# Kernel tuning notes

Hardware: AMD Instinct MI355X
Metric: run time of the kernel (lower is better)

## Reference

```python
import jax, jax.numpy as jnp
import numpy as np

EPS = 1e-5

def setup_inputs() -> dict:
    key = jax.random.key(0)
    k1, k2, k3 = jax.random.split(key, 3)
    x = jax.random.normal(k1, (16, 256, 32, 32), dtype=jnp.float32)
    embed = jax.random.normal(k2, (8192, 256), dtype=jnp.float32)
    cluster_size = jax.random.uniform(k3, (8192,), dtype=jnp.float32)
    return {"x": x, "embed": embed, "cluster_size": cluster_size}

def reference(x, embed, cluster_size):
    # x: (b, c, h, w) -> (b, h*w, c); project_in is Identity (codebook_dim == dim, heads=1)
    b, c, h, w = x.shape
    xt = jnp.transpose(x, (0, 2, 3, 1)).reshape(b, h * w, c)   # (b, n, d)
    flat = xt.reshape(-1, c)                                    # (N, d)
    d2 = (jnp.sum(flat * flat, axis=1, keepdims=True)
          - 2.0 * flat @ embed.T
          + jnp.sum(embed * embed, axis=1))                     # (N, K)
    embed_ind_flat = jnp.argmin(d2, axis=-1)                    # (N,) temperature==0 -> argmax of -d2
    quantize = embed[embed_ind_flat].reshape(b, h * w, c)       # gather codebook rows
    embed_ind = embed_ind_flat.reshape(b, h * w)
    # perplexity over (unnormalized) EMA cluster sizes, as in the torch code
    probs = cluster_size
    perplexity = jnp.exp(-jnp.sum(probs * jnp.log(probs + EPS)))
    # eval-mode commitment loss (weight_loss=True, commitment_weight=1.0)
    commit_loss = jnp.mean((quantize - xt) ** 2)
    return quantize, embed_ind, perplexity, commit_loss
```

## Files before the change

kernel.cpp:

```cpp
#include <hip/hip_runtime.h>
#include <hip/hip_bf16.h>
#include <math.h>

typedef _Float16 f16x8 __attribute__((ext_vector_type(8)));
typedef float f32x4 __attribute__((ext_vector_type(4)));

#define N_TOK 16384
#define D 256
#define K 8192

#define Q_OFF 0
#define IND_OFF 4194304
#define PERP_OFF 4210688
#define COMMIT_OFF 4210689

#define WS_CAND   0u
#define WS_E2     1048576u
#define WS_DSUM   1081344u
#define WS_EH     1114112u
#define WS_XH     5308416u
#define WS_XT     13697024u
#define WS_NEED   30474240u

__device__ __forceinline__ unsigned int ford(float f) {
    unsigned int u = __float_as_uint(f);
    return (u & 0x80000000u) ? ~u : (u | 0x80000000u);
}
__device__ __forceinline__ unsigned short f2h(float f) {
    _Float16 h = (_Float16)f;
    return *(unsigned short*)&h;
}


__global__ void vq_convert_x(const float* __restrict__ x, float* __restrict__ xt,
                             unsigned short* __restrict__ xh) {
    __shared__ float t[64][65];
    const int tid = threadIdx.x;
    const int p0 = blockIdx.x * 64, c0 = blockIdx.y * 64, b = blockIdx.z;
    const int q = tid & 15, h = tid >> 4;
    #pragma unroll
    for (int r = 0; r < 4; ++r) {
        const int cl = r * 16 + h;
        const float4 v = *(const float4*)(x + (((size_t)(b * 256 + c0 + cl)) << 10) + p0 + q * 4);
        t[cl][q * 4 + 0] = v.x; t[cl][q * 4 + 1] = v.y;
        t[cl][q * 4 + 2] = v.z; t[cl][q * 4 + 3] = v.w;
    }
    __syncthreads();
    #pragma unroll
    for (int r = 0; r < 4; ++r) {
        const int nl = r * 16 + h;
        const int n = (b << 10) + p0 + nl;
        const int c = c0 + q * 4;
        float4 vf; ushort4 vh;
        vf.x = t[q * 4 + 0][nl]; vf.y = t[q * 4 + 1][nl];
        vf.z = t[q * 4 + 2][nl]; vf.w = t[q * 4 + 3][nl];
        vh.x = f2h(vf.x); vh.y = f2h(vf.y); vh.z = f2h(vf.z); vh.w = f2h(vf.w);
        *(float4*)(xt + ((size_t)n << 8) + c) = vf;
        *(ushort4*)(xh + ((size_t)n << 8) + c) = vh;
    }
}

__global__ void vq_prep_e(const float* __restrict__ e, unsigned short* __restrict__ ehT,
                          float* __restrict__ e2, double* __restrict__ dsum) {
    if (blockIdx.x == 0 && threadIdx.x == 0) *dsum = 0.0;
    const int wave = threadIdx.x >> 6, lane = threadIdx.x & 63;
    const int c = blockIdx.x * 4 + wave;
    const float4 v = *(const float4*)(e + (size_t)c * D + lane * 4);
    ushort4 vh;
    vh.x = f2h(v.x); vh.y = f2h(v.y); vh.z = f2h(v.z); vh.w = f2h(v.w);
    unsigned short* dst = ehT + (((size_t)(c >> 4)) << 12) + ((lane >> 1) << 7) +
                          ((c & 15) << 3) + ((lane & 1) << 2);
    *(ushort4*)dst = vh;
    float s = v.x * v.x + v.y * v.y + v.z * v.z + v.w * v.w;
    #pragma unroll
    for (int off = 32; off > 0; off >>= 1) s += __shfl_down(s, off, 64);
    if (lane == 0) e2[c] = s;
}

__global__ __launch_bounds__(256)
void vq_mfma_kernel(
    const unsigned short* __restrict__ xh, const unsigned short* __restrict__ ehT,
    const float* __restrict__ e2, unsigned int* __restrict__ cand) {
    __shared__ float e2s[1024];

    const int tid = threadIdx.x;
    const int lane = tid & 63, wid = tid >> 6;
    const int l15 = lane & 15, lg = lane >> 4;
    const int split = blockIdx.y;
    const int m0 = blockIdx.x * 128;
    const int c0s = split * 1024;
    const int rw = m0 + wid * 32;

    {
        float4 v = *(const float4*)(e2 + c0s + tid * 4);
        v.x += 512.0f; v.y += 512.0f; v.z += 512.0f; v.w += 512.0f;
        *(float4*)&e2s[tid * 4] = v;
    }

    f16x8 a[2][8];
    #pragma unroll
    for (int mf = 0; mf < 2; ++mf) {
        const unsigned short* ap = xh + (((size_t)(rw + mf * 16 + l15)) << 8) + lg * 8;
        #pragma unroll
        for (int t = 0; t < 8; ++t)
            a[mf][t] = *(const f16x8*)(ap + t * 32);
    }
    __syncthreads();

    const char* bb = (const char*)ehT + (((size_t)c0s) << 9) + lane * 16;

    unsigned int p1[8], p2[8];
    #pragma unroll
    for (int r = 0; r < 8; ++r) { p1[r] = 0xFFFFFFFFu; p2[r] = 0xFFFFFFFFu; }

    f16x8 bA[8], bB[8];
    f32x4 accA[2], accB[2];

#define LOADT(breg, t)                                            \
    {                                                             \
        const char* tb_ = bb + (t) * 8192;                        \
        _Pragma("unroll")                                         \
        for (int j_ = 0; j_ < 8; ++j_)                            \
            breg[j_] = *(const f16x8*)(tb_ + j_ * 1024);          \
    }

#define MFMAT(acc, breg)                                          \
    {                                                             \
        _Pragma("unroll")                                         \
        for (int mf_ = 0; mf_ < 2; ++mf_) {                       \
            f32x4 z_ = {0.f, 0.f, 0.f, 0.f};                      \
            acc[mf_] = z_;                                        \
        }                                                         \
        _Pragma("unroll")                                         \
        for (int j_ = 0; j_ < 8; ++j_)                            \
            _Pragma("unroll")                                     \
            for (int mf_ = 0; mf_ < 2; ++mf_)                     \
                acc[mf_] = __builtin_amdgcn_mfma_f32_16x16x32_f16(\
                    a[mf_][j_], breg[j_], acc[mf_], 0, 0, 0);     \
    }

#define EPI(acc, tile)                                                        \
    {                                                                         \
        const float e2v_ = e2s[(tile) * 16 + l15];                            \
        const unsigned int cl_ = (unsigned int)((tile) * 16 + l15);           \
        _Pragma("unroll")                                                     \
        for (int mf_ = 0; mf_ < 2; ++mf_)                                     \
            _Pragma("unroll")                                                 \
            for (int rg_ = 0; rg_ < 4; ++rg_) {                               \
                const int rr_ = mf_ * 4 + rg_;                                \
                const float s_ = fmaf(-2.0f, acc[mf_][rg_], e2v_);            \
                const unsigned int sp_ =                                      \
                    (__float_as_uint(s_) & 0xFFFFFC00u) | cl_;                \
                const unsigned int hi_ = p1[rr_] > sp_ ? p1[rr_] : sp_;       \
                p1[rr_] = p1[rr_] < sp_ ? p1[rr_] : sp_;                      \
                p2[rr_] = p2[rr_] < hi_ ? p2[rr_] : hi_;                      \
            }                                                                 \
    }

    LOADT(bA, 0);
    #pragma unroll 1
    for (int t = 0; t < 64; t += 2) {
        LOADT(bB, t + 1);
        MFMAT(accA, bA);
        if (t > 0) EPI(accB, t - 1);
        if (t + 2 < 64) LOADT(bA, t + 2);
        MFMAT(accB, bB);
        EPI(accA, t);
    }
    EPI(accB, 63);

    #pragma unroll
    for (int st = 1; st < 16; st <<= 1) {
        #pragma unroll
        for (int r = 0; r < 8; ++r) {
            const unsigned int q1 = (unsigned int)__shfl_xor((int)p1[r], st, 64);
            const unsigned int q2 = (unsigned int)__shfl_xor((int)p2[r], st, 64);
            const unsigned int n1 = p1[r] < q1 ? p1[r] : q1;
            const unsigned int hi = p1[r] < q1 ? q1 : p1[r];
            const unsigned int m2 = p2[r] < q2 ? p2[r] : q2;
            p1[r] = n1;
            p2[r] = m2 < hi ? m2 : hi;
        }
    }
    if (l15 == 0) {
        #pragma unroll
        for (int mf = 0; mf < 2; ++mf)
            #pragma unroll
            for (int reg = 0; reg < 4; ++reg) {
                const int rr = mf * 4 + reg;
                const int n = rw + mf * 16 + lg * 4 + reg;
                unsigned int* cp = cand + (((size_t)n) << 4) + split * 2;
                cp[0] = (unsigned int)(c0s + (p1[rr] & 0x3FFu));
                cp[1] = (unsigned int)(c0s + (p2[rr] & 0x3FFu));
            }
    }
#undef LOADT
#undef MFMAT
#undef EPI
}

__global__ void vq_rescore_finalize(const float* __restrict__ xt, const float* __restrict__ embed,
                                    const float* __restrict__ e2,
                                    const unsigned int* __restrict__ cand,
                                    float* __restrict__ out, double* __restrict__ dsum) {
    __shared__ double red[4];
    const int tid = threadIdx.x, wid = tid >> 6, lane = tid & 63;
    double wsum = 0.0;
    #pragma unroll 1
    for (int it = 0; it < 4; ++it) {
        const int n = blockIdx.x * 16 + it * 4 + wid;
        const float4 xv = *(const float4*)(xt + (((size_t)n) << 8) + lane * 4);
        unsigned long long best = 0xFFFFFFFFFFFFFFFFull;
        #pragma unroll 2
        for (int j = 0; j < 16; ++j) {
            const unsigned int c = cand[(((size_t)n) << 4) + j];
            const float4 ev = *(const float4*)(embed + (((size_t)c) << 8) + lane * 4);
            float dt = xv.x * ev.x + xv.y * ev.y + xv.z * ev.z + xv.w * ev.w;
            #pragma unroll
            for (int off = 32; off > 0; off >>= 1) dt += __shfl_xor(dt, off, 64);
            const float s = fmaf(-2.0f, dt, e2[c]);
            const unsigned long long p = (((unsigned long long)ford(s)) << 32) | c;
            best = p < best ? p : best;
        }
        const unsigned int bi = (unsigned int)(best & 0xFFFFFFFFull);
        if (lane == 0) out[IND_OFF + n] = (float)bi;
        const float4 ev = *(const float4*)(embed + (((size_t)bi) << 8) + lane * 4);
        *(float4*)(out + Q_OFF + (((size_t)n) << 8) + lane * 4) = ev;
        const float q0 = ev.x - xv.x, q1 = ev.y - xv.y, q2 = ev.z - xv.z, q3 = ev.w - xv.w;
        float a4 = q0 * q0 + q1 * q1 + q2 * q2 + q3 * q3;
        #pragma unroll
        for (int off = 32; off > 0; off >>= 1) a4 += __shfl_xor(a4, off, 64);
        if (lane == 0) wsum += (double)a4;
    }
    if (lane == 0) red[wid] = wsum;
    __syncthreads();
    if (tid == 0) atomicAdd(dsum, red[0] + red[1] + red[2] + red[3]);
}

__global__ void vq_tail_kernel(const float* __restrict__ cs,
                               const double* __restrict__ dsum,
                               float* __restrict__ out) {
    __shared__ double red[4];
    const int tid = threadIdx.x;
    double s = 0.0;
    for (int i = tid; i < K; i += 256) {
        const float p = cs[i];
        s += (double)(p * logf(p + 1e-5f));
    }
    #pragma unroll
    for (int off = 32; off > 0; off >>= 1) s += __shfl_down(s, off, 64);
    if ((tid & 63) == 0) red[tid >> 6] = s;
    __syncthreads();
    if (tid == 0) {
        const double tot = red[0] + red[1] + red[2] + red[3];
        const double pv = exp(-tot);
        out[PERP_OFF] = (pv > 3.3e38) ? 3.3e38f : (float)pv;
        out[COMMIT_OFF] = (float)(*dsum * (1.0 / 4194304.0));
    }
}

#define TM 64
#define TN 64
#define BKF 32
#define NSPLITF 2
#define CODES_PER_SPLIT (K / NSPLITF)
#define TILES_PER_SPLIT (CODES_PER_SPLIT / TN)

__global__ void vq_init_kernel(unsigned long long* __restrict__ keys, double* __restrict__ dsum) {
    int i = blockIdx.x * blockDim.x + threadIdx.x;
    if (i < N_TOK) keys[i] = 0xFFFFFFFFFFFFFFFFull;
    if (i == 0) *dsum = 0.0;
}
__global__ void vq_e2_kernel(const float* __restrict__ embed, float* __restrict__ e2) {
    int wave = threadIdx.x >> 6, lane = threadIdx.x & 63;
    int c = blockIdx.x * 4 + wave;
    const float4 v = *(const float4*)(embed + (size_t)c * D + lane * 4);
    float s = v.x * v.x + v.y * v.y + v.z * v.z + v.w * v.w;
    #pragma unroll
    for (int off = 32; off > 0; off >>= 1) s += __shfl_down(s, off, 64);
    if (lane == 0) e2[c] = s;
}
__global__ __launch_bounds__(256, 2) void vq_argmin_kernel(
    const float* __restrict__ x, const float* __restrict__ embed,
    const float* __restrict__ e2, unsigned long long* __restrict__ keys) {
    __shared__ float xT[D][TM];
    __shared__ float eT[BKF][TN + 4];
    const int tid = threadIdx.x;
    const int n0 = blockIdx.x * TM;
    const int b = n0 >> 10, p0 = n0 & 1023;
    const float* xb = x + (size_t)b * D * 1024 + p0;
    {
        const int t4 = (tid & 15) * 4, chb = tid >> 4;
        #pragma unroll
        for (int pass = 0; pass < 16; ++pass) {
            const int ch = pass * 16 + chb;
            *(float4*)&xT[ch][t4] = *(const float4*)(xb + (size_t)ch * 1024 + t4);
        }
    }
    __syncthreads();
    const int tm4 = (tid & 15) * 4, tn = tid >> 4, tn4 = tn * 4;
    float bestd[4]; int besti[4];
    #pragma unroll
    for (int i = 0; i < 4; ++i) { bestd[i] = INFINITY; besti[i] = 0x7fffffff; }
    for (int ct = 0; ct < TILES_PER_SPLIT; ++ct) {
        const int c0 = blockIdx.y * CODES_PER_SPLIT + ct * TN;
        float acc[4][4] = {};
        for (int kk = 0; kk < D; kk += BKF) {
            {
                const int j = tid >> 2, ch4 = (tid & 3) * 4;
                #pragma unroll
                for (int p = 0; p < 2; ++p) {
                    const int chl = p * 16 + ch4;
                    const float4 ev = *(const float4*)(embed + (size_t)(c0 + j) * D + kk + chl);
                    eT[chl + 0][j] = ev.x; eT[chl + 1][j] = ev.y;
                    eT[chl + 2][j] = ev.z; eT[chl + 3][j] = ev.w;
                }
            }
            __syncthreads();
            #pragma unroll
            for (int k2 = 0; k2 < BKF; ++k2) {
                const float4 a = *(const float4*)&xT[kk + k2][tm4];
                const float4 bv = *(const float4*)&eT[k2][tn4];
                acc[0][0] += a.x * bv.x; acc[0][1] += a.x * bv.y; acc[0][2] += a.x * bv.z; acc[0][3] += a.x * bv.w;
                acc[1][0] += a.y * bv.x; acc[1][1] += a.y * bv.y; acc[1][2] += a.y * bv.z; acc[1][3] += a.y * bv.w;
                acc[2][0] += a.z * bv.x; acc[2][1] += a.z * bv.y; acc[2][2] += a.z * bv.z; acc[2][3] += a.z * bv.w;
                acc[3][0] += a.w * bv.x; acc[3][1] += a.w * bv.y; acc[3][2] += a.w * bv.z; acc[3][3] += a.w * bv.w;
            }
            __syncthreads();
        }
        #pragma unroll
        for (int j = 0; j < 4; ++j) {
            const int c = c0 + tn4 + j;
            const float ec = e2[c];
            #pragma unroll
            for (int i = 0; i < 4; ++i) {
                const float s = ec - 2.0f * acc[i][j];
                if (s < bestd[i]) { bestd[i] = s; besti[i] = c; }
            }
        }
    }
    __syncthreads();
    float* cd = &eT[0][0];
    int* ci = (int*)&eT[16][0];
    #pragma unroll
    for (int i = 0; i < 4; ++i) { cd[tn * 64 + tm4 + i] = bestd[i]; ci[tn * 64 + tm4 + i] = besti[i]; }
    __syncthreads();
    if (tid < TM) {
        float bd = INFINITY; int bi = 0x7fffffff;
        for (int j = 0; j < 16; ++j) {
            const float d = cd[j * 64 + tid]; const int idx = ci[j * 64 + tid];
            if (d < bd || (d == bd && idx < bi)) { bd = d; bi = idx; }
        }
        atomicMin(&keys[n0 + tid], (((unsigned long long)ford(bd)) << 32) | (unsigned int)bi);
    }
}
__global__ void vq_finalize_kernel(const float* __restrict__ x, const float* __restrict__ embed,
                                   const unsigned long long* __restrict__ keys,
                                   float* __restrict__ out, double* __restrict__ dsum) {
    const int tid = threadIdx.x;
    const int n0 = blockIdx.x * 64;
    const int t = tid >> 2, q = tid & 3;
    const int n = n0 + t;
    const int b = n >> 10, p = n & 1023;
    if (tid < 64) {
        const int nn = n0 + tid;
        out[IND_OFF + nn] = (float)(int)(unsigned int)(keys[nn] & 0xFFFFFFFFull);
    }
    const int idx = (int)(unsigned int)(keys[n] & 0xFFFFFFFFull);
    const float* erow = embed + (size_t)idx * D;
    const float* xrow = x + (size_t)b * D * 1024 + p;
    float* qrow = out + Q_OFF + (size_t)n * D;
    float acc = 0.0f;
    #pragma unroll
    for (int i = 0; i < 16; ++i) {
        const int ch = i * 16 + q * 4;
        const float4 ev = *(const float4*)(erow + ch);
        *(float4*)(qrow + ch) = ev;
        const float x0 = xrow[(size_t)(ch + 0) * 1024];
        const float x1 = xrow[(size_t)(ch + 1) * 1024];
        const float x2 = xrow[(size_t)(ch + 2) * 1024];
        const float x3 = xrow[(size_t)(ch + 3) * 1024];
        const float d0 = ev.x - x0, d1 = ev.y - x1, d2 = ev.z - x2, d3 = ev.w - x3;
        acc += d0 * d0 + d1 * d1 + d2 * d2 + d3 * d3;
    }
    #pragma unroll
    for (int off = 32; off > 0; off >>= 1) acc += __shfl_down(acc, off, 64);
    if ((tid & 63) == 0) atomicAdd(dsum, (double)acc);
}

extern "C" void kernel_launch(void* const* d_in, const int* in_sizes, int n_in,
                              void* d_out, int out_size, void* d_ws, size_t ws_size,
                              hipStream_t stream) {
    const float* x = (const float*)d_in[0];
    const float* embed = (const float*)d_in[1];
    const float* cs = (const float*)d_in[2];
    float* out = (float*)d_out;
    char* ws = (char*)d_ws;

    if (ws_size >= (size_t)WS_NEED) {
        unsigned int* cand = (unsigned int*)(ws + WS_CAND);
        float* e2 = (float*)(ws + WS_E2);
        double* dsum = (double*)(ws + WS_DSUM);
        unsigned short* ehT = (unsigned short*)(ws + WS_EH);
        unsigned short* xh = (unsigned short*)(ws + WS_XH);
        float* xt = (float*)(ws + WS_XT);

        vq_prep_e<<<dim3(K / 4), dim3(256), 0, stream>>>(embed, ehT, e2, dsum);
        vq_convert_x<<<dim3(16, 4, 16), dim3(256), 0, stream>>>(x, xt, xh);
        vq_mfma_kernel<<<dim3(128, 8), dim3(256), 0, stream>>>(xh, ehT, e2, cand);
        vq_rescore_finalize<<<dim3(1024), dim3(256), 0, stream>>>(xt, embed, e2, cand, out, dsum);
        vq_tail_kernel<<<dim3(1), dim3(256), 0, stream>>>(cs, dsum, out);
    } else {
        unsigned long long* keys = (unsigned long long*)ws;
        float* e2 = (float*)(ws + 131072);
        double* dsum = (double*)(ws + 163840);
        vq_init_kernel<<<dim3(64), dim3(256), 0, stream>>>(keys, dsum);
        vq_e2_kernel<<<dim3(K / 4), dim3(256), 0, stream>>>(embed, e2);
        vq_argmin_kernel<<<dim3(N_TOK / TM, NSPLITF), dim3(256), 0, stream>>>(x, embed, e2, keys);
        vq_finalize_kernel<<<dim3(256), dim3(256), 0, stream>>>(x, embed, keys, out, dsum);
        vq_tail_kernel<<<dim3(1), dim3(256), 0, stream>>>(cs, dsum, out);
    }
}
```

Baseline: 157.7 us.

## Merge prep kernels and fold tail reduction into rescore via ticket

Merges the embedding prep, x transpose/convert and perplexity computation into one launch using block-index ranges. It drops the separate tail kernel by having the last rescore block, found through an atomic ticket counter, write the commit loss. It also halves the tokens per rescore block and doubles the grid for more parallelism. This cuts two kernel launches and their gaps, at the cost of an extra atomic per block and a tail-block dependence on a correct memory fence.

```diff
diff --git a/kernel.cpp b/kernel.cpp
--- a/kernel.cpp
+++ b/kernel.cpp
@@ -17,6 +17,7 @@
 #define WS_CAND   0u
 #define WS_E2     1048576u
 #define WS_DSUM   1081344u
+#define WS_TICK   1081352u
 #define WS_EH     1114112u
 #define WS_XH     5308416u
 #define WS_XT     13697024u
@@ -32,49 +33,71 @@
 }
 
 
-__global__ void vq_convert_x(const float* __restrict__ x, float* __restrict__ xt,
-                             unsigned short* __restrict__ xh) {
+__global__ void vq_prep(const float* __restrict__ x, const float* __restrict__ embed,
+                        const float* __restrict__ cs,
+                        float* __restrict__ xt, unsigned short* __restrict__ xh,
+                        unsigned short* __restrict__ ehT, float* __restrict__ e2,
+                        double* __restrict__ dsum, unsigned int* __restrict__ ticket,
+                        float* __restrict__ out) {
     __shared__ float t[64][65];
+    const int bid = blockIdx.x;
     const int tid = threadIdx.x;
-    const int p0 = blockIdx.x * 64, c0 = blockIdx.y * 64, b = blockIdx.z;
-    const int q = tid & 15, h = tid >> 4;
-    #pragma unroll
-    for (int r = 0; r < 4; ++r) {
-        const int cl = r * 16 + h;
-        const float4 v = *(const float4*)(x + (((size_t)(b * 256 + c0 + cl)) << 10) + p0 + q * 4);
-        t[cl][q * 4 + 0] = v.x; t[cl][q * 4 + 1] = v.y;
-        t[cl][q * 4 + 2] = v.z; t[cl][q * 4 + 3] = v.w;
-    }
-    __syncthreads();
-    #pragma unroll
-    for (int r = 0; r < 4; ++r) {
-        const int nl = r * 16 + h;
-        const int n = (b << 10) + p0 + nl;
-        const int c = c0 + q * 4;
-        float4 vf; ushort4 vh;
-        vf.x = t[q * 4 + 0][nl]; vf.y = t[q * 4 + 1][nl];
-        vf.z = t[q * 4 + 2][nl]; vf.w = t[q * 4 + 3][nl];
-        vh.x = f2h(vf.x); vh.y = f2h(vf.y); vh.z = f2h(vf.z); vh.w = f2h(vf.w);
-        *(float4*)(xt + ((size_t)n << 8) + c) = vf;
-        *(ushort4*)(xh + ((size_t)n << 8) + c) = vh;
-    }
-}
-
-__global__ void vq_prep_e(const float* __restrict__ e, unsigned short* __restrict__ ehT,
-                          float* __restrict__ e2, double* __restrict__ dsum) {
-    if (blockIdx.x == 0 && threadIdx.x == 0) *dsum = 0.0;
-    const int wave = threadIdx.x >> 6, lane = threadIdx.x & 63;
-    const int c = blockIdx.x * 4 + wave;
-    const float4 v = *(const float4*)(e + (size_t)c * D + lane * 4);
-    ushort4 vh;
-    vh.x = f2h(v.x); vh.y = f2h(v.y); vh.z = f2h(v.z); vh.w = f2h(v.w);
-    unsigned short* dst = ehT + (((size_t)(c >> 4)) << 12) + ((lane >> 1) << 7) +
-                          ((c & 15) << 3) + ((lane & 1) << 2);
-    *(ushort4*)dst = vh;
-    float s = v.x * v.x + v.y * v.y + v.z * v.z + v.w * v.w;
-    #pragma unroll
-    for (int off = 32; off > 0; off >>= 1) s += __shfl_down(s, off, 64);
-    if (lane == 0) e2[c] = s;
+
+    if (bid < 2048) {
+        if (bid == 0 && tid == 0) { *dsum = 0.0; *ticket = 0u; }
+        const int wave = tid >> 6, lane = tid & 63;
+        const int c = bid * 4 + wave;
+        const float4 v = *(const float4*)(embed + (size_t)c * D + lane * 4);
+        ushort4 vh;
+        vh.x = f2h(v.x); vh.y = f2h(v.y); vh.z = f2h(v.z); vh.w = f2h(v.w);
+        unsigned short* dst = ehT + (((size_t)(c >> 4)) << 12) + ((lane >> 1) << 7) +
+                              ((c & 15) << 3) + ((lane & 1) << 2);
+        *(ushort4*)dst = vh;
+        float s = v.x * v.x + v.y * v.y + v.z * v.z + v.w * v.w;
+        #pragma unroll
+        for (int off = 32; off > 0; off >>= 1) s += __shfl_down(s, off, 64);
+        if (lane == 0) e2[c] = s;
+    } else if (bid < 3072) {
+        const int i = bid - 2048;
+        const int p0 = (i & 15) * 64, c0 = ((i >> 4) & 3) * 64, b = i >> 6;
+        const int q = tid & 15, h = tid >> 4;
+        #pragma unroll
+        for (int r = 0; r < 4; ++r) {
+            const int cl = r * 16 + h;
+            const float4 v = *(const float4*)(x + (((size_t)(b * 256 + c0 + cl)) << 10) + p0 + q * 4);
+            t[cl][q * 4 + 0] = v.x; t[cl][q * 4 + 1] = v.y;
+            t[cl][q * 4 + 2] = v.z; t[cl][q * 4 + 3] = v.w;
+        }
+        __syncthreads();
+        #pragma unroll
+        for (int r = 0; r < 4; ++r) {
+            const int nl = r * 16 + h;
+            const int n = (b << 10) + p0 + nl;
+            const int c = c0 + q * 4;
+            float4 vf; ushort4 vh;
+            vf.x = t[q * 4 + 0][nl]; vf.y = t[q * 4 + 1][nl];
+            vf.z = t[q * 4 + 2][nl]; vf.w = t[q * 4 + 3][nl];
+            vh.x = f2h(vf.x); vh.y = f2h(vf.y); vh.z = f2h(vf.z); vh.w = f2h(vf.w);
+            *(float4*)(xt + ((size_t)n << 8) + c) = vf;
+            *(ushort4*)(xh + ((size_t)n << 8) + c) = vh;
+        }
+    } else {
+        double* red = (double*)&t[0][0];
+        double s = 0.0;
+        for (int i2 = tid; i2 < K; i2 += 256) {
+            const float p = cs[i2];
+            s += (double)(p * logf(p + 1e-5f));
+        }
+        #pragma unroll
+        for (int off = 32; off > 0; off >>= 1) s += __shfl_down(s, off, 64);
+        if ((tid & 63) == 0) red[tid >> 6] = s;
+        __syncthreads();
+        if (tid == 0) {
+            const double tot = red[0] + red[1] + red[2] + red[3];
+            const double pv = exp(-tot);
+            out[PERP_OFF] = (pv > 3.3e38) ? 3.3e38f : (float)pv;
+        }
+    }
 }
 
 __global__ __launch_bounds__(256)
@@ -202,13 +225,14 @@
 __global__ void vq_rescore_finalize(const float* __restrict__ xt, const float* __restrict__ embed,
                                     const float* __restrict__ e2,
                                     const unsigned int* __restrict__ cand,
-                                    float* __restrict__ out, double* __restrict__ dsum) {
+                                    float* __restrict__ out, double* __restrict__ dsum,
+                                    unsigned int* __restrict__ ticket) {
     __shared__ double red[4];
     const int tid = threadIdx.x, wid = tid >> 6, lane = tid & 63;
     double wsum = 0.0;
     #pragma unroll 1
-    for (int it = 0; it < 4; ++it) {
-        const int n = blockIdx.x * 16 + it * 4 + wid;
+    for (int it = 0; it < 2; ++it) {
+        const int n = blockIdx.x * 8 + it * 4 + wid;
         const float4 xv = *(const float4*)(xt + (((size_t)n) << 8) + lane * 4);
         unsigned long long best = 0xFFFFFFFFFFFFFFFFull;
         #pragma unroll 2
@@ -234,8 +258,23 @@
     }
     if (lane == 0) red[wid] = wsum;
     __syncthreads();
-    if (tid == 0) atomicAdd(dsum, red[0] + red[1] + red[2] + red[3]);
-}
+    if (tid == 0) {
+        atomicAdd(dsum, red[0] + red[1] + red[2] + red[3]);
+        __threadfence();
+        const unsigned int tk = atomicAdd(ticket, 1u);
+        if (tk == gridDim.x - 1) {
+            const double total = atomicAdd(dsum, 0.0);
+            out[COMMIT_OFF] = (float)(total * (1.0 / 4194304.0));
+        }
+    }
+}
+
+#define TM 64
+#define TN 64
+#define BKF 32
+#define NSPLITF 2
+#define CODES_PER_SPLIT (K / NSPLITF)
+#define TILES_PER_SPLIT (CODES_PER_SPLIT / TN)
 
 __global__ void vq_tail_kernel(const float* __restrict__ cs,
                                const double* __restrict__ dsum,
@@ -258,13 +297,6 @@
         out[COMMIT_OFF] = (float)(*dsum * (1.0 / 4194304.0));
     }
 }
-
-#define TM 64
-#define TN 64
-#define BKF 32
-#define NSPLITF 2
-#define CODES_PER_SPLIT (K / NSPLITF)
-#define TILES_PER_SPLIT (CODES_PER_SPLIT / TN)
 
 __global__ void vq_init_kernel(unsigned long long* __restrict__ keys, double* __restrict__ dsum) {
     int i = blockIdx.x * blockDim.x + threadIdx.x;
@@ -401,15 +433,16 @@
         unsigned int* cand = (unsigned int*)(ws + WS_CAND);
         float* e2 = (float*)(ws + WS_E2);
         double* dsum = (double*)(ws + WS_DSUM);
+        unsigned int* ticket = (unsigned int*)(ws + WS_TICK);
         unsigned short* ehT = (unsigned short*)(ws + WS_EH);
         unsigned short* xh = (unsigned short*)(ws + WS_XH);
         float* xt = (float*)(ws + WS_XT);
 
-        vq_prep_e<<<dim3(K / 4), dim3(256), 0, stream>>>(embed, ehT, e2, dsum);
-        vq_convert_x<<<dim3(16, 4, 16), dim3(256), 0, stream>>>(x, xt, xh);
+        vq_prep<<<dim3(3073), dim3(256), 0, stream>>>(x, embed, cs, xt, xh, ehT, e2,
+                                                      dsum, ticket, out);
         vq_mfma_kernel<<<dim3(128, 8), dim3(256), 0, stream>>>(xh, ehT, e2, cand);
-        vq_rescore_finalize<<<dim3(1024), dim3(256), 0, stream>>>(xt, embed, e2, cand, out, dsum);
-        vq_tail_kernel<<<dim3(1), dim3(256), 0, stream>>>(cs, dsum, out);
+        vq_rescore_finalize<<<dim3(2048), dim3(256), 0, stream>>>(xt, embed, e2, cand,
+                                                                  out, dsum, ticket);
     } else {
         unsigned long long* keys = (unsigned long long*)ws;
         float* e2 = (float*)(ws + 131072);
```

Measured after the change: 190.0 us. 20.5% more time.
